# Kernel optimization log

Measured on AMD Instinct MI355X. Metric: run time of the kernel, lower is better.

## Reference

```python
import jax, jax.numpy as jnp
import numpy as np

N_EMBED = 768
NUM_EXPERTS = 8
TOP_K = 2
B, S = 2, 2048
THRESH = 1e-09


def setup_inputs() -> dict:
    key = jax.random.key(0)
    ks = jax.random.split(key, 12)
    d, e, f = N_EMBED, NUM_EXPERTS, 4 * N_EMBED
    s_in = 1.0 / np.sqrt(d)
    s_hid = 1.0 / np.sqrt(f)
    return {
        'x': jax.random.normal(ks[0], (B, S, d), jnp.float32),
        'noise': jax.random.normal(ks[1], (B * S, e), jnp.float32),
        'Wg': jax.random.normal(ks[2], (d, e), jnp.float32) * s_in,
        'bg': jnp.zeros((e,), jnp.float32),
        'Wn': jax.random.normal(ks[3], (d, e), jnp.float32) * s_in,
        'bn': jnp.zeros((e,), jnp.float32),
        'W1': jax.random.normal(ks[4], (e, d, f), jnp.float32) * s_in,
        'b1': jnp.zeros((e, f), jnp.float32),
        'W2': jax.random.normal(ks[5], (e, f, d), jnp.float32) * s_hid,
        'b2': jnp.zeros((e, d), jnp.float32),
    }


def reference(x, noise, Wg, bg, Wn, bn, W1, b1, W2, b2):
    Bsz, Ssz, d = x.shape
    T = Bsz * Ssz
    xr = x.reshape(T, d)  # [T, d]

    # Noisy top-k router
    logits = xr @ Wg + bg                     # [T, E]
    noise_logits = xr @ Wn + bn               # [T, E]
    noisy = logits + noise * jax.nn.softplus(noise_logits)
    vals, idx = jax.lax.top_k(noisy, TOP_K)   # [T, K]
    rows = jnp.arange(T)[:, None]
    sparse = jnp.full_like(noisy, -jnp.inf).at[rows, idx].set(vals)
    probs = jax.nn.softmax(sparse, axis=-1)   # [T, E]; zeros off top-k

    # Gate = prob masked by activation threshold (matches torch dispatch)
    gate = jnp.where(probs > THRESH, probs, 0.0)  # [T, E]

    # Dense per-expert MLP (dropout=0 -> identity), combined by gate
    h = jax.nn.relu(jnp.einsum('td,edf->etf', xr, W1) + b1[:, None, :])  # [E, T, 4d]
    y = jnp.einsum('etf,efd->etd', h, W2) + b2[:, None, :]               # [E, T, d]
    out = jnp.einsum('te,etd->td', gate, y)                              # [T, d]
    return out.reshape(Bsz, Ssz, d)
```

## Files before the change

### kernel.cpp

```cpp
#include <hip/hip_runtime.h>
#include <math.h>

typedef unsigned short u16;
typedef unsigned int u32;

#define D_EMB 768
#define F_HID 3072
#define N_TOK 4096
#define N_PAIR 8192
#define GATE_TH 1e-9f

typedef float f32x4 __attribute__((ext_vector_type(4)));
typedef __bf16 bfrag __attribute__((ext_vector_type(8)));

__device__ inline float b2f(u16 u) {
    union { float f; u32 i; } c; c.i = ((u32)u) << 16; return c.f;
}
__device__ inline u16 f2b(float f) {
    union { float f; u32 i; } c; c.f = f;
    u32 r = c.i + 0x7FFFu + ((c.i >> 16) & 1u);
    return (u16)(r >> 16);
}
__device__ inline f32x4 mfma16(bfrag a, bfrag b, f32x4 c) {
    return __builtin_amdgcn_mfma_f32_16x16x32_bf16(a, b, c, 0, 0, 0);
}
__device__ inline void gll16(const u16* g, u16* l) {
    __builtin_amdgcn_global_load_lds(
        (const __attribute__((address_space(1))) u32*)g,
        (__attribute__((address_space(3))) u32*)l, 16, 0, 0);
}
__device__ inline void sbar() {
    asm volatile("" ::: "memory");
    __builtin_amdgcn_s_barrier();
    asm volatile("" ::: "memory");
}
__device__ inline void waitv0() { asm volatile("s_waitcnt vmcnt(0)" ::: "memory"); }
__device__ inline void waitv6() { asm volatile("s_waitcnt vmcnt(6)" ::: "memory"); }
__device__ inline void waitv8() { asm volatile("s_waitcnt vmcnt(8)" ::: "memory"); }

__global__ void moe_init_kernel(int* __restrict__ cnt) {
    if (threadIdx.x < 8) cnt[threadIdx.x] = 0;
}
__global__ __launch_bounds__(256) void moe_zero_kernel(uint4* __restrict__ out) {
    int i = blockIdx.x * 256 + threadIdx.x;
    out[i] = make_uint4(0, 0, 0, 0);
}

__global__ __launch_bounds__(64) void moe_router_v2(
    const float* __restrict__ x, const float* __restrict__ noise,
    const float* __restrict__ Wg, const float* __restrict__ bg,
    const float* __restrict__ Wn, const float* __restrict__ bn,
    int* __restrict__ tk_e, float* __restrict__ tk_g, int* __restrict__ cnt)
{
    const int lane = threadIdx.x;
    const int tl = lane & 7, q = lane >> 3;
    const int t = blockIdx.x * 8 + tl;
    float ag[8] = {}, an[8] = {};
    const float4* xp = (const float4*)(x + (size_t)t * D_EMB + q * 96);
#pragma unroll 4
    for (int k4 = 0; k4 < 24; k4++) {
        float4 xv = xp[k4];
        const int kb = q * 96 + k4 * 4;
#pragma unroll
        for (int c = 0; c < 4; c++) {
            float xc = (&xv.x)[c];
            const float4* wg = (const float4*)(Wg + (size_t)(kb + c) * 8);
            const float4* wn = (const float4*)(Wn + (size_t)(kb + c) * 8);
            float4 g0 = wg[0], g1 = wg[1], n0 = wn[0], n1 = wn[1];
            ag[0] += xc * g0.x; ag[1] += xc * g0.y; ag[2] += xc * g0.z; ag[3] += xc * g0.w;
            ag[4] += xc * g1.x; ag[5] += xc * g1.y; ag[6] += xc * g1.z; ag[7] += xc * g1.w;
            an[0] += xc * n0.x; an[1] += xc * n0.y; an[2] += xc * n0.z; an[3] += xc * n0.w;
            an[4] += xc * n1.x; an[5] += xc * n1.y; an[6] += xc * n1.z; an[7] += xc * n1.w;
        }
    }
#pragma unroll
    for (int e = 0; e < 8; e++) {
        ag[e] += __shfl_xor(ag[e], 8);  an[e] += __shfl_xor(an[e], 8);
        ag[e] += __shfl_xor(ag[e], 16); an[e] += __shfl_xor(an[e], 16);
        ag[e] += __shfl_xor(ag[e], 32); an[e] += __shfl_xor(an[e], 32);
    }
    if (q == 0) {
        float best = -INFINITY, sec = -INFINITY; int be = 0, se = 0;
#pragma unroll
        for (int e = 0; e < 8; e++) {
            float nl = an[e] + bn[e];
            float sp = nl > 0.f ? nl + log1pf(expf(-nl)) : log1pf(expf(nl));
            float v = ag[e] + bg[e] + noise[(size_t)t * 8 + e] * sp;
            if (v > best) { sec = best; se = be; best = v; be = e; }
            else if (v > sec) { sec = v; se = e; }
        }
        float ex = expf(sec - best);
        float g1 = 1.f / (1.f + ex), g2 = ex / (1.f + ex);
        tk_e[t * 2 + 0] = (g1 > GATE_TH) ? be : -1; tk_g[t * 2 + 0] = g1;
        tk_e[t * 2 + 1] = (g2 > GATE_TH) ? se : -1; tk_g[t * 2 + 1] = g2;
        if (g1 > GATE_TH) atomicAdd(&cnt[be], 1);
        if (g2 > GATE_TH) atomicAdd(&cnt[se], 1);
    }
}

__global__ void moe_offsets_kernel(const int* __restrict__ cnt,
                                   int* __restrict__ off, int* __restrict__ cursor) {
    if (threadIdx.x == 0) {
        int s = 0;
        for (int e = 0; e < 8; e++) { off[e] = s; cursor[e] = s; s += cnt[e]; }
    }
}
__global__ void moe_scatter_kernel(const int* __restrict__ tk_e, const float* __restrict__ tk_g,
                                   int* __restrict__ cursor, int* __restrict__ plist,
                                   float* __restrict__ pg, int* __restrict__ pos) {
    int i = blockIdx.x * 256 + threadIdx.x;
    if (i < N_PAIR) {
        int e = tk_e[i];
        if (e >= 0) {
            int p = atomicAdd(&cursor[e], 1);
            plist[p] = i >> 1;
            pg[p] = tk_g[i];
            pos[i] = p;
        }
    }
}

__global__ __launch_bounds__(256) void moe_cvtx_kernel(
    const float4* __restrict__ x, ushort4* __restrict__ xb) {
    int i = blockIdx.x * 256 + threadIdx.x;
    float4 v = x[i];
    ushort4 o;
    o.x = f2b(v.x); o.y = f2b(v.y); o.z = f2b(v.z); o.w = f2b(v.w);
    xb[i] = o;
}

__global__ __launch_bounds__(256) void moe_transcvt_kernel(
    const float* __restrict__ in, u16* __restrict__ out, int R, int C) {
    __shared__ float tile[32][33];
    const int z = blockIdx.z;
    const int c0 = blockIdx.x * 32, r0 = blockIdx.y * 32;
    const int tx = threadIdx.x & 31, ty = threadIdx.x >> 5;
    const size_t base = (size_t)z * R * C;
#pragma unroll
    for (int j = 0; j < 32; j += 8)
        tile[ty + j][tx] = in[base + (size_t)(r0 + ty + j) * C + c0 + tx];
    __syncthreads();
#pragma unroll
    for (int j = 0; j < 32; j += 8)
        out[base + (size_t)(c0 + ty + j) * R + r0 + tx] = f2b(tile[tx][ty + j]);
}

__global__ __launch_bounds__(256) void moe_ffn1_kernel(
    const u16* __restrict__ xb, const u16* __restrict__ w1t, const float* __restrict__ b1,
    const int* __restrict__ plist, const int* __restrict__ cnt, const int* __restrict__ off,
    u16* __restrict__ h, int P0, int P1)
{
    __shared__ __align__(16) u16 As[2][128 * 64];
    __shared__ __align__(16) u16 Bs[2][128 * 64];
    const int GX = 24, GY = 16;
    int f = blockIdx.x + GX * (blockIdx.y + GY * blockIdx.z);
    int swz = (f & 7) * 384 + (f >> 3);
    int nb = swz % GX;
    int t2 = swz / GX;
    int mb = t2 % GY;
    int e  = t2 / GY;

    int lo = off[e], hi = lo + cnt[e];
    if (lo < P0) lo = P0;
    if (hi > P1) hi = P1;
    const int Cl = hi - lo;
    if (Cl <= 0) return;
    const int n0 = nb * 128;
    const int tid = threadIdx.x;
    const int lane = tid & 63, wave = tid >> 6;
    const int wr = wave >> 1, wc = wave & 1;
    const int qq = lane >> 4, r = lane & 15;
    const int srow = tid >> 3;
    const int gq = (tid & 7) ^ (srow & 7);

    const u16* bsrc[4];
#pragma unroll
    for (int j = 0; j < 4; j++)
        bsrc[j] = w1t + ((size_t)e * F_HID + n0 + j * 32 + srow) * D_EMB + gq * 8;

    for (int m0 = mb * 128; m0 < Cl; m0 += GY * 128) {
        const u16* asrc[4];
#pragma unroll
        for (int j = 0; j < 4; j++) {
            int mr = m0 + j * 32 + srow;
            if (mr > Cl - 1) mr = Cl - 1;
            asrc[j] = xb + (size_t)plist[lo + mr] * D_EMB + gq * 8;
        }
        f32x4 acc[4][4] = {};

        auto stage = [&](int kt, int buf) {
            const int k0 = kt * 64;
#pragma unroll
            for (int j = 0; j < 4; j++)
                gll16(asrc[j] + k0, &As[buf][j * 2048 + wave * 512]);
#pragma unroll
            for (int j = 0; j < 4; j++)
                gll16(bsrc[j] + k0, &Bs[buf][j * 2048 + wave * 512]);
        };
        auto compute = [&](int buf) {
#pragma unroll
            for (int kk = 0; kk < 2; kk++) {
                bfrag af[4], bf[4];
#pragma unroll
                for (int i = 0; i < 4; i++) {
                    int rowa = wr * 64 + i * 16 + r;
                    int rowb = wc * 64 + i * 16 + r;
                    int slot = ((qq + 4 * kk) ^ (r & 7)) * 8;
                    af[i] = *(const bfrag*)(&As[buf][rowa * 64 + slot]);
                    bf[i] = *(const bfrag*)(&Bs[buf][rowb * 64 + slot]);
                }
#pragma unroll
                for (int mi = 0; mi < 4; mi++)
#pragma unroll
                    for (int ni = 0; ni < 4; ni++)
                        acc[mi][ni] = mfma16(af[mi], bf[ni], acc[mi][ni]);
            }
        };

        waitv0();
        stage(0, 0);
        for (int kt = 0; kt < 11; kt++) {
            stage(kt + 1, (kt + 1) & 1);
            waitv8(); sbar();
            compute(kt & 1);
            sbar();
        }
        waitv0(); sbar();
        compute(1);

#pragma unroll
        for (int mi = 0; mi < 4; mi++)
#pragma unroll
            for (int ni = 0; ni < 4; ni++) {
                int col = n0 + wc * 64 + ni * 16 + r;
                float bias = b1[(size_t)e * F_HID + col];
#pragma unroll
                for (int i = 0; i < 4; i++) {
                    int m = m0 + wr * 64 + mi * 16 + qq * 4 + i;
                    if (m < Cl) {
                        float v = acc[mi][ni][i] + bias;
                        h[(size_t)(lo - P0 + m) * F_HID + col] = f2b(v > 0.f ? v : 0.f);
                    }
                }
            }
    }
}

__global__ __launch_bounds__(256) void moe_ffn2_kernel(
    const u16* __restrict__ h, const u16* __restrict__ w2t, const float* __restrict__ b2,
    const int* __restrict__ cnt, const int* __restrict__ off,
    float* __restrict__ y, int P0, int P1)
{
    __shared__ __align__(16) u16 As[2][64 * 64];
    __shared__ __align__(16) u16 Bs[2][128 * 64];
    const int GX = 6, GY = 32;
    int f = blockIdx.x + GX * (blockIdx.y + GY * blockIdx.z);
    int swz = (f & 7) * 192 + (f >> 3);
    int nb = swz % GX;
    int t2 = swz / GX;
    int mb = t2 % GY;
    int e  = t2 / GY;

    int lo = off[e], hi = lo + cnt[e];
    if (lo < P0) lo = P0;
    if (hi > P1) hi = P1;
    const int Cl = hi - lo;
    if (Cl <= 0) return;
    const int n0 = nb * 128;
    const int tid = threadIdx.x;
    const int lane = tid & 63, wave = tid >> 6;
    const int wr = wave >> 1, wc = wave & 1;
    const int qq = lane >> 4, r = lane & 15;
    const int srow = tid >> 3;
    const int gq = (tid & 7) ^ (srow & 7);
    const int hcap = P1 - P0;

    const u16* bsrc[4];
#pragma unroll
    for (int j = 0; j < 4; j++)
        bsrc[j] = w2t + ((size_t)e * D_EMB + n0 + j * 32 + srow) * F_HID + gq * 8;

    for (int m0 = mb * 64; m0 < Cl; m0 += GY * 64) {
        const u16* asrc[2];
#pragma unroll
        for (int j = 0; j < 2; j++) {
            int mr = m0 + j * 32 + srow;
            if (mr > Cl - 1) mr = Cl - 1;
            asrc[j] = h + (size_t)(lo - P0 + ((mr < hcap) ? mr : hcap - 1)) * F_HID + gq * 8;
        }
        f32x4 acc[2][4] = {};

        auto stage = [&](int kt, int buf) {
            const int k0 = kt * 64;
#pragma unroll
            for (int j = 0; j < 2; j++)
                gll16(asrc[j] + k0, &As[buf][j * 2048 + wave * 512]);
#pragma unroll
            for (int j = 0; j < 4; j++)
                gll16(bsrc[j] + k0, &Bs[buf][j * 2048 + wave * 512]);
        };
        auto compute = [&](int buf) {
#pragma unroll
            for (int kk = 0; kk < 2; kk++) {
                bfrag af[2], bf[4];
#pragma unroll
                for (int i = 0; i < 2; i++) {
                    int rowa = wr * 32 + i * 16 + r;
                    int slot = ((qq + 4 * kk) ^ (r & 7)) * 8;
                    af[i] = *(const bfrag*)(&As[buf][rowa * 64 + slot]);
                }
#pragma unroll
                for (int i = 0; i < 4; i++) {
                    int rowb = wc * 64 + i * 16 + r;
                    int slot = ((qq + 4 * kk) ^ (r & 7)) * 8;
                    bf[i] = *(const bfrag*)(&Bs[buf][rowb * 64 + slot]);
                }
#pragma unroll
                for (int mi = 0; mi < 2; mi++)
#pragma unroll
                    for (int ni = 0; ni < 4; ni++)
                        acc[mi][ni] = mfma16(af[mi], bf[ni], acc[mi][ni]);
            }
        };

        waitv0();
        stage(0, 0);
        for (int kt = 0; kt < 47; kt++) {
            stage(kt + 1, (kt + 1) & 1);
            waitv6(); sbar();
            compute(kt & 1);
            sbar();
        }
        waitv0(); sbar();
        compute(1);

#pragma unroll
        for (int mi = 0; mi < 2; mi++)
#pragma unroll
            for (int ni = 0; ni < 4; ni++) {
                int col = n0 + wc * 64 + ni * 16 + r;
                float bias = b2[(size_t)e * D_EMB + col];
#pragma unroll
                for (int i = 0; i < 4; i++) {
                    int m = m0 + wr * 32 + mi * 16 + qq * 4 + i;
                    if (m < Cl)
                        y[(size_t)(lo + m) * D_EMB + col] = acc[mi][ni][i] + bias;
                }
            }
    }
}

__global__ __launch_bounds__(256) void moe_combine_kernel(
    const float* __restrict__ y, const int* __restrict__ tk_e,
    const float* __restrict__ tk_g, const int* __restrict__ pos,
    float4* __restrict__ out)
{
    int i = blockIdx.x * 256 + threadIdx.x;
    int t = i / 192;
    int c = i - t * 192;
    float4 a = make_float4(0.f, 0.f, 0.f, 0.f);
#pragma unroll
    for (int k = 0; k < 2; k++) {
        int e = tk_e[t * 2 + k];
        if (e >= 0) {
            float g = tk_g[t * 2 + k];
            float4 v = ((const float4*)(y + (size_t)pos[t * 2 + k] * D_EMB))[c];
            a.x += g * v.x; a.y += g * v.y; a.z += g * v.z; a.w += g * v.w;
        }
    }
    out[i] = a;
}

#define XSTR 776
#define HSTR 3080
#define BMF 8
__global__ __launch_bounds__(256) void moe_ffn_fused_f32(
    const float* __restrict__ x,
    const float* __restrict__ w1, const float* __restrict__ b1,
    const float* __restrict__ w2, const float* __restrict__ b2,
    const int* __restrict__ plist, const float* __restrict__ pg,
    const int* __restrict__ cnt, const int* __restrict__ off,
    float* __restrict__ out)
{
    __shared__ __align__(16) u16 xs[BMF * XSTR];
    __shared__ __align__(16) u16 hs[BMF * HSTR];
    const int e = blockIdx.x;
    const int Cl = cnt[e];
    if (Cl <= 0) return;
    const int O = off[e];
    const int tid = threadIdx.x;
    for (int t0 = blockIdx.y * BMF; t0 < Cl; t0 += gridDim.y * BMF) {
        for (int ci = tid; ci < BMF * 192; ci += 256) {
            int row = ci / 192, c = ci - row * 192;
            float4 v = make_float4(0.f, 0.f, 0.f, 0.f);
            if (t0 + row < Cl) {
                int tok = plist[O + t0 + row];
                v = *(const float4*)(x + (size_t)tok * D_EMB + c * 4);
            }
            u16* d = &xs[row * XSTR + c * 4];
            d[0] = f2b(v.x); d[1] = f2b(v.y); d[2] = f2b(v.z); d[3] = f2b(v.w);
        }
        __syncthreads();
        for (int wi = tid; wi < BMF * 768; wi += 256) {
            int row = wi / 768, nc = wi - row * 768;
            int n0 = nc * 4;
            float a0 = 0, a1 = 0, a2 = 0, a3 = 0;
            const float* wp = w1 + (size_t)e * D_EMB * F_HID + n0;
            const u16* xr = &xs[row * XSTR];
            for (int k = 0; k < D_EMB; k++) {
                float4 wv = *(const float4*)(wp + (size_t)k * F_HID);
                float xv = b2f(xr[k]);
                a0 += xv * wv.x; a1 += xv * wv.y; a2 += xv * wv.z; a3 += xv * wv.w;
            }
            const float* bp = b1 + (size_t)e * F_HID + n0;
            u16* hp = &hs[row * HSTR + n0];
            float v;
            v = a0 + bp[0]; hp[0] = f2b(v > 0.f ? v : 0.f);
            v = a1 + bp[1]; hp[1] = f2b(v > 0.f ? v : 0.f);
            v = a2 + bp[2]; hp[2] = f2b(v > 0.f ? v : 0.f);
            v = a3 + bp[3]; hp[3] = f2b(v > 0.f ? v : 0.f);
        }
        __syncthreads();
        for (int wi = tid; wi < BMF * 192; wi += 256) {
            int row = wi / 192, nc = wi - row * 192;
            int n0 = nc * 4;
            float a0 = 0, a1 = 0, a2 = 0, a3 = 0;
            const float* wp = w2 + (size_t)e * F_HID * D_EMB + n0;
            const u16* hr = &hs[row * HSTR];
            for (int k = 0; k < F_HID; k++) {
                float4 wv = *(const float4*)(wp + (size_t)k * D_EMB);
                float hv = b2f(hr[k]);
                a0 += hv * wv.x; a1 += hv * wv.y; a2 += hv * wv.z; a3 += hv * wv.w;
            }
            if (t0 + row < Cl) {
                int p = O + t0 + row;
                int tok = plist[p];
                float g = pg[p];
                const float* bp = b2 + (size_t)e * D_EMB + n0;
                float* op = out + (size_t)tok * D_EMB + n0;
                atomicAdd(&op[0], g * (a0 + bp[0]));
                atomicAdd(&op[1], g * (a1 + bp[1]));
                atomicAdd(&op[2], g * (a2 + bp[2]));
                atomicAdd(&op[3], g * (a3 + bp[3]));
            }
        }
        __syncthreads();
    }
}

extern "C" void kernel_launch(void* const* d_in, const int* in_sizes, int n_in,
                              void* d_out, int out_size, void* d_ws, size_t ws_size,
                              hipStream_t stream) {
    const float* x     = (const float*)d_in[0];
    const float* noise = (const float*)d_in[1];
    const float* Wg    = (const float*)d_in[2];
    const float* bg    = (const float*)d_in[3];
    const float* Wn    = (const float*)d_in[4];
    const float* bn    = (const float*)d_in[5];
    const float* W1    = (const float*)d_in[6];
    const float* b1    = (const float*)d_in[7];
    const float* W2    = (const float*)d_in[8];
    const float* b2    = (const float*)d_in[9];
    float* out = (float*)d_out;

    char* ws = (char*)d_ws;
    int*   cnt    = (int*)(ws + 0);
    int*   off    = (int*)(ws + 256);
    int*   cursor = (int*)(ws + 512);
    int*   tk_e   = (int*)(ws + 1024);
    float* tk_g   = (float*)(ws + 33792);
    int*   plist  = (int*)(ws + 66560);
    float* pg     = (float*)(ws + 99328);
    int*   pos    = (int*)(ws + 132096);
    const size_t W1T_OFF = 164864;
    const size_t W2T_OFF = W1T_OFF + 37748736ull;
    const size_t XB_OFF  = W2T_OFF + 37748736ull;
    const size_t Y_OFF   = XB_OFF + 6291456ull;
    const size_t H_OFF   = Y_OFF + 25165824ull;
    u16*   w1t = (u16*)(ws + W1T_OFF);
    u16*   w2t = (u16*)(ws + W2T_OFF);
    u16*   xb  = (u16*)(ws + XB_OFF);
    float* y   = (float*)(ws + Y_OFF);
    u16*   h   = (u16*)(ws + H_OFF);

    int pchunk = 0;
    for (int p = N_PAIR; p >= 512; p >>= 1) {
        if (H_OFF + (size_t)p * F_HID * 2 <= ws_size) { pchunk = p; break; }
    }

    moe_init_kernel<<<dim3(1), dim3(64), 0, stream>>>(cnt);
    moe_router_v2<<<dim3(512), dim3(64), 0, stream>>>(
        x, noise, Wg, bg, Wn, bn, tk_e, tk_g, cnt);
    moe_offsets_kernel<<<dim3(1), dim3(64), 0, stream>>>(cnt, off, cursor);
    moe_scatter_kernel<<<dim3(N_PAIR / 256), dim3(256), 0, stream>>>(
        tk_e, tk_g, cursor, plist, pg, pos);

    if (pchunk > 0) {
        moe_cvtx_kernel<<<dim3(3072), dim3(256), 0, stream>>>(
            (const float4*)x, (ushort4*)xb);
        moe_transcvt_kernel<<<dim3(F_HID / 32, D_EMB / 32, 8), dim3(256), 0, stream>>>(
            W1, w1t, D_EMB, F_HID);
        moe_transcvt_kernel<<<dim3(D_EMB / 32, F_HID / 32, 8), dim3(256), 0, stream>>>(
            W2, w2t, F_HID, D_EMB);
        for (int c = 0; c < N_PAIR / pchunk; c++) {
            int P0 = c * pchunk, P1 = P0 + pchunk;
            moe_ffn1_kernel<<<dim3(24, 16, 8), dim3(256), 0, stream>>>(
                xb, w1t, b1, plist, cnt, off, h, P0, P1);
            moe_ffn2_kernel<<<dim3(6, 32, 8), dim3(256), 0, stream>>>(
                h, w2t, b2, cnt, off, y, P0, P1);
        }
        moe_combine_kernel<<<dim3(3072), dim3(256), 0, stream>>>(
            y, tk_e, tk_g, pos, (float4*)out);
    } else {
        moe_zero_kernel<<<dim3(3072), dim3(256), 0, stream>>>((uint4*)out);
        moe_ffn_fused_f32<<<dim3(8, 192), dim3(256), 0, stream>>>(
            x, W1, b1, W2, b2, plist, pg, cnt, off, out);
    }
    (void)in_sizes; (void)n_in; (void)out_size;
}
```

Measured before the change: 462.9 us.

## Shrink GEMM K-tile to 32, enlarge FFN2 M-tile, fuse x cast into router

Both expert GEMM kernels now stage 32-wide K slices instead of 64, using a new XOR swizzle and smaller LDS buffers. FFN2 moves to 128x128 tiles with 16 M-blocks. The bf16 cast of x is folded into the router kernel, and when the workspace is large enough a single weight buffer is shared: W1 is transposed, FFN1 runs, then W2 is transposed into the same buffer, all without chunking. The goal is higher occupancy, less LDS pressure and fewer launches, at the cost of twice as many barriers per K step and weight transposes that no longer overlap.

```diff
diff --git a/kernel.cpp b/kernel.cpp
--- a/kernel.cpp
+++ b/kernel.cpp
@@ -35,8 +35,7 @@
     asm volatile("" ::: "memory");
 }
 __device__ inline void waitv0() { asm volatile("s_waitcnt vmcnt(0)" ::: "memory"); }
-__device__ inline void waitv6() { asm volatile("s_waitcnt vmcnt(6)" ::: "memory"); }
-__device__ inline void waitv8() { asm volatile("s_waitcnt vmcnt(8)" ::: "memory"); }
+__device__ inline void waitv4() { asm volatile("s_waitcnt vmcnt(4)" ::: "memory"); }
 
 __global__ void moe_init_kernel(int* __restrict__ cnt) {
     if (threadIdx.x < 8) cnt[threadIdx.x] = 0;
@@ -46,11 +45,12 @@
     out[i] = make_uint4(0, 0, 0, 0);
 }
 
-__global__ __launch_bounds__(64) void moe_router_v2(
+__global__ __launch_bounds__(64) void moe_router_v3(
     const float* __restrict__ x, const float* __restrict__ noise,
     const float* __restrict__ Wg, const float* __restrict__ bg,
     const float* __restrict__ Wn, const float* __restrict__ bn,
-    int* __restrict__ tk_e, float* __restrict__ tk_g, int* __restrict__ cnt)
+    int* __restrict__ tk_e, float* __restrict__ tk_g, int* __restrict__ cnt,
+    ushort4* __restrict__ xb4)
 {
     const int lane = threadIdx.x;
     const int tl = lane & 7, q = lane >> 3;
@@ -95,6 +95,16 @@
         tk_e[t * 2 + 1] = (g2 > GATE_TH) ? se : -1; tk_g[t * 2 + 1] = g2;
         if (g1 > GATE_TH) atomicAdd(&cnt[be], 1);
         if (g2 > GATE_TH) atomicAdd(&cnt[se], 1);
+    }
+    if (xb4) {
+        const int t0 = blockIdx.x * 8;
+        for (int i = lane; i < 8 * 192; i += 64) {
+            int ti = i / 192, c = i - ti * 192;
+            float4 v = *(const float4*)(x + (size_t)(t0 + ti) * D_EMB + c * 4);
+            ushort4 o;
+            o.x = f2b(v.x); o.y = f2b(v.y); o.z = f2b(v.z); o.w = f2b(v.w);
+            xb4[(size_t)(t0 + ti) * 192 + c] = o;
+        }
     }
 }
 
@@ -120,15 +130,6 @@
     }
 }
 
-__global__ __launch_bounds__(256) void moe_cvtx_kernel(
-    const float4* __restrict__ x, ushort4* __restrict__ xb) {
-    int i = blockIdx.x * 256 + threadIdx.x;
-    float4 v = x[i];
-    ushort4 o;
-    o.x = f2b(v.x); o.y = f2b(v.y); o.z = f2b(v.z); o.w = f2b(v.w);
-    xb[i] = o;
-}
-
 __global__ __launch_bounds__(256) void moe_transcvt_kernel(
     const float* __restrict__ in, u16* __restrict__ out, int R, int C) {
     __shared__ float tile[32][33];
@@ -146,12 +147,12 @@
 }
 
 __global__ __launch_bounds__(256) void moe_ffn1_kernel(
-    const u16* __restrict__ xb, const u16* __restrict__ w1t, const float* __restrict__ b1,
+    const u16* __restrict__ xb, const u16* __restrict__ wt, const float* __restrict__ b1,
     const int* __restrict__ plist, const int* __restrict__ cnt, const int* __restrict__ off,
     u16* __restrict__ h, int P0, int P1)
 {
-    __shared__ __align__(16) u16 As[2][128 * 64];
-    __shared__ __align__(16) u16 Bs[2][128 * 64];
+    __shared__ __align__(16) u16 As[2][128 * 32];
+    __shared__ __align__(16) u16 Bs[2][128 * 32];
     const int GX = 24, GY = 16;
     int f = blockIdx.x + GX * (blockIdx.y + GY * blockIdx.z);
     int swz = (f & 7) * 384 + (f >> 3);
@@ -170,58 +171,55 @@
     const int lane = tid & 63, wave = tid >> 6;
     const int wr = wave >> 1, wc = wave & 1;
     const int qq = lane >> 4, r = lane & 15;
-    const int srow = tid >> 3;
-    const int gq = (tid & 7) ^ (srow & 7);
-
-    const u16* bsrc[4];
-#pragma unroll
-    for (int j = 0; j < 4; j++)
-        bsrc[j] = w1t + ((size_t)e * F_HID + n0 + j * 32 + srow) * D_EMB + gq * 8;
+    const int sig = (r & 3) ^ ((r >> 2) & 3);
+    const int sa = ((qq ^ sig) << 3);
+    const int srow = tid >> 2;
+    const int gq = (tid & 3) ^ ((tid >> 2) & 3) ^ ((tid >> 4) & 3);
+
+    const u16* bsrc[2];
+#pragma unroll
+    for (int j = 0; j < 2; j++)
+        bsrc[j] = wt + ((size_t)e * F_HID + n0 + j * 64 + srow) * D_EMB + gq * 8;
 
     for (int m0 = mb * 128; m0 < Cl; m0 += GY * 128) {
-        const u16* asrc[4];
-#pragma unroll
-        for (int j = 0; j < 4; j++) {
-            int mr = m0 + j * 32 + srow;
+        const u16* asrc[2];
+#pragma unroll
+        for (int j = 0; j < 2; j++) {
+            int mr = m0 + j * 64 + srow;
             if (mr > Cl - 1) mr = Cl - 1;
             asrc[j] = xb + (size_t)plist[lo + mr] * D_EMB + gq * 8;
         }
         f32x4 acc[4][4] = {};
 
         auto stage = [&](int kt, int buf) {
-            const int k0 = kt * 64;
-#pragma unroll
-            for (int j = 0; j < 4; j++)
+            const int k0 = kt * 32;
+#pragma unroll
+            for (int j = 0; j < 2; j++)
                 gll16(asrc[j] + k0, &As[buf][j * 2048 + wave * 512]);
 #pragma unroll
-            for (int j = 0; j < 4; j++)
+            for (int j = 0; j < 2; j++)
                 gll16(bsrc[j] + k0, &Bs[buf][j * 2048 + wave * 512]);
         };
         auto compute = [&](int buf) {
-#pragma unroll
-            for (int kk = 0; kk < 2; kk++) {
-                bfrag af[4], bf[4];
-#pragma unroll
-                for (int i = 0; i < 4; i++) {
-                    int rowa = wr * 64 + i * 16 + r;
-                    int rowb = wc * 64 + i * 16 + r;
-                    int slot = ((qq + 4 * kk) ^ (r & 7)) * 8;
-                    af[i] = *(const bfrag*)(&As[buf][rowa * 64 + slot]);
-                    bf[i] = *(const bfrag*)(&Bs[buf][rowb * 64 + slot]);
-                }
-#pragma unroll
-                for (int mi = 0; mi < 4; mi++)
-#pragma unroll
-                    for (int ni = 0; ni < 4; ni++)
-                        acc[mi][ni] = mfma16(af[mi], bf[ni], acc[mi][ni]);
-            }
+            bfrag af[4], bf[4];
+#pragma unroll
+            for (int i = 0; i < 4; i++) {
+                af[i] = *(const bfrag*)(&As[buf][(wr * 64 + i * 16 + r) * 32 + sa]);
+                bf[i] = *(const bfrag*)(&Bs[buf][(wc * 64 + i * 16 + r) * 32 + sa]);
+            }
+#pragma unroll
+            for (int mi = 0; mi < 4; mi++)
+#pragma unroll
+                for (int ni = 0; ni < 4; ni++)
+                    acc[mi][ni] = mfma16(af[mi], bf[ni], acc[mi][ni]);
         };
 
         waitv0();
         stage(0, 0);
-        for (int kt = 0; kt < 11; kt++) {
+#pragma unroll 2
+        for (int kt = 0; kt < 23; kt++) {
             stage(kt + 1, (kt + 1) & 1);
-            waitv8(); sbar();
+            waitv4(); sbar();
             compute(kt & 1);
             sbar();
         }
@@ -243,19 +241,20 @@
                     }
                 }
             }
+        sbar();
     }
 }
 
 __global__ __launch_bounds__(256) void moe_ffn2_kernel(
-    const u16* __restrict__ h, const u16* __restrict__ w2t, const float* __restrict__ b2,
+    const u16* __restrict__ h, const u16* __restrict__ wt, const float* __restrict__ b2,
     const int* __restrict__ cnt, const int* __restrict__ off,
     float* __restrict__ y, int P0, int P1)
 {
-    __shared__ __align__(16) u16 As[2][64 * 64];
-    __shared__ __align__(16) u16 Bs[2][128 * 64];
-    const int GX = 6, GY = 32;
+    __shared__ __align__(16) u16 As[2][128 * 32];
+    __shared__ __align__(16) u16 Bs[2][128 * 32];
+    const int GX = 6, GY = 16;
     int f = blockIdx.x + GX * (blockIdx.y + GY * blockIdx.z);
-    int swz = (f & 7) * 192 + (f >> 3);
+    int swz = (f & 7) * 96 + (f >> 3);
     int nb = swz % GX;
     int t2 = swz / GX;
     int mb = t2 % GY;
@@ -271,63 +270,55 @@
     const int lane = tid & 63, wave = tid >> 6;
     const int wr = wave >> 1, wc = wave & 1;
     const int qq = lane >> 4, r = lane & 15;
-    const int srow = tid >> 3;
-    const int gq = (tid & 7) ^ (srow & 7);
-    const int hcap = P1 - P0;
-
-    const u16* bsrc[4];
-#pragma unroll
-    for (int j = 0; j < 4; j++)
-        bsrc[j] = w2t + ((size_t)e * D_EMB + n0 + j * 32 + srow) * F_HID + gq * 8;
-
-    for (int m0 = mb * 64; m0 < Cl; m0 += GY * 64) {
+    const int sig = (r & 3) ^ ((r >> 2) & 3);
+    const int sa = ((qq ^ sig) << 3);
+    const int srow = tid >> 2;
+    const int gq = (tid & 3) ^ ((tid >> 2) & 3) ^ ((tid >> 4) & 3);
+
+    const u16* bsrc[2];
+#pragma unroll
+    for (int j = 0; j < 2; j++)
+        bsrc[j] = wt + ((size_t)e * D_EMB + n0 + j * 64 + srow) * F_HID + gq * 8;
+
+    for (int m0 = mb * 128; m0 < Cl; m0 += GY * 128) {
         const u16* asrc[2];
 #pragma unroll
         for (int j = 0; j < 2; j++) {
-            int mr = m0 + j * 32 + srow;
+            int mr = m0 + j * 64 + srow;
             if (mr > Cl - 1) mr = Cl - 1;
-            asrc[j] = h + (size_t)(lo - P0 + ((mr < hcap) ? mr : hcap - 1)) * F_HID + gq * 8;
-        }
-        f32x4 acc[2][4] = {};
+            asrc[j] = h + (size_t)(lo - P0 + mr) * F_HID + gq * 8;
+        }
+        f32x4 acc[4][4] = {};
 
         auto stage = [&](int kt, int buf) {
-            const int k0 = kt * 64;
+            const int k0 = kt * 32;
 #pragma unroll
             for (int j = 0; j < 2; j++)
                 gll16(asrc[j] + k0, &As[buf][j * 2048 + wave * 512]);
 #pragma unroll
-            for (int j = 0; j < 4; j++)
+            for (int j = 0; j < 2; j++)
                 gll16(bsrc[j] + k0, &Bs[buf][j * 2048 + wave * 512]);
         };
         auto compute = [&](int buf) {
-#pragma unroll
-            for (int kk = 0; kk < 2; kk++) {
-                bfrag af[2], bf[4];
-#pragma unroll
-                for (int i = 0; i < 2; i++) {
-                    int rowa = wr * 32 + i * 16 + r;
-                    int slot = ((qq + 4 * kk) ^ (r & 7)) * 8;
-                    af[i] = *(const bfrag*)(&As[buf][rowa * 64 + slot]);
-                }
-#pragma unroll
-                for (int i = 0; i < 4; i++) {
-                    int rowb = wc * 64 + i * 16 + r;
-                    int slot = ((qq + 4 * kk) ^ (r & 7)) * 8;
-                    bf[i] = *(const bfrag*)(&Bs[buf][rowb * 64 + slot]);
-                }
-#pragma unroll
-                for (int mi = 0; mi < 2; mi++)
-#pragma unroll
-                    for (int ni = 0; ni < 4; ni++)
-                        acc[mi][ni] = mfma16(af[mi], bf[ni], acc[mi][ni]);
-            }
+            bfrag af[4], bf[4];
+#pragma unroll
+            for (int i = 0; i < 4; i++) {
+                af[i] = *(const bfrag*)(&As[buf][(wr * 64 + i * 16 + r) * 32 + sa]);
+                bf[i] = *(const bfrag*)(&Bs[buf][(wc * 64 + i * 16 + r) * 32 + sa]);
+            }
+#pragma unroll
+            for (int mi = 0; mi < 4; mi++)
+#pragma unroll
+                for (int ni = 0; ni < 4; ni++)
+                    acc[mi][ni] = mfma16(af[mi], bf[ni], acc[mi][ni]);
         };
 
         waitv0();
         stage(0, 0);
-        for (int kt = 0; kt < 47; kt++) {
+#pragma unroll 2
+        for (int kt = 0; kt < 95; kt++) {
             stage(kt + 1, (kt + 1) & 1);
-            waitv6(); sbar();
+            waitv4(); sbar();
             compute(kt & 1);
             sbar();
         }
@@ -335,18 +326,19 @@
         compute(1);
 
 #pragma unroll
-        for (int mi = 0; mi < 2; mi++)
+        for (int mi = 0; mi < 4; mi++)
 #pragma unroll
             for (int ni = 0; ni < 4; ni++) {
                 int col = n0 + wc * 64 + ni * 16 + r;
                 float bias = b2[(size_t)e * D_EMB + col];
 #pragma unroll
                 for (int i = 0; i < 4; i++) {
-                    int m = m0 + wr * 32 + mi * 16 + qq * 4 + i;
+                    int m = m0 + wr * 64 + mi * 16 + qq * 4 + i;
                     if (m < Cl)
                         y[(size_t)(lo + m) * D_EMB + col] = acc[mi][ni][i] + bias;
                 }
             }
+        sbar();
     }
 }
 
@@ -472,32 +464,60 @@
     int*   plist  = (int*)(ws + 66560);
     float* pg     = (float*)(ws + 99328);
     int*   pos    = (int*)(ws + 132096);
-    const size_t W1T_OFF = 164864;
-    const size_t W2T_OFF = W1T_OFF + 37748736ull;
-    const size_t XB_OFF  = W2T_OFF + 37748736ull;
-    const size_t Y_OFF   = XB_OFF + 6291456ull;
-    const size_t H_OFF   = Y_OFF + 25165824ull;
-    u16*   w1t = (u16*)(ws + W1T_OFF);
-    u16*   w2t = (u16*)(ws + W2T_OFF);
-    u16*   xb  = (u16*)(ws + XB_OFF);
-    float* y   = (float*)(ws + Y_OFF);
-    u16*   h   = (u16*)(ws + H_OFF);
-
+    const size_t SMALL  = 164864;
+    const size_t WSZ    = 37748736ull;
+    const size_t XB_SZ  = 6291456ull;
+    const size_t Y_SZ   = 25165824ull;
+    const size_t H_FULL = 50331648ull;
+
+    const size_t NEED_A = SMALL + WSZ + XB_SZ + Y_SZ + H_FULL;
+
+    if (ws_size >= NEED_A) {
+        u16*   wt = (u16*)(ws + SMALL);
+        u16*   xb = (u16*)(ws + SMALL + WSZ);
+        float* y  = (float*)(ws + SMALL + WSZ + XB_SZ);
+        u16*   h  = (u16*)(ws + SMALL + WSZ + XB_SZ + Y_SZ);
+
+        moe_init_kernel<<<dim3(1), dim3(64), 0, stream>>>(cnt);
+        moe_router_v3<<<dim3(512), dim3(64), 0, stream>>>(
+            x, noise, Wg, bg, Wn, bn, tk_e, tk_g, cnt, (ushort4*)xb);
+        moe_offsets_kernel<<<dim3(1), dim3(64), 0, stream>>>(cnt, off, cursor);
+        moe_scatter_kernel<<<dim3(N_PAIR / 256), dim3(256), 0, stream>>>(
+            tk_e, tk_g, cursor, plist, pg, pos);
+        moe_transcvt_kernel<<<dim3(F_HID / 32, D_EMB / 32, 8), dim3(256), 0, stream>>>(
+            W1, wt, D_EMB, F_HID);
+        moe_ffn1_kernel<<<dim3(24, 16, 8), dim3(256), 0, stream>>>(
+            xb, wt, b1, plist, cnt, off, h, 0, N_PAIR);
+        moe_transcvt_kernel<<<dim3(D_EMB / 32, F_HID / 32, 8), dim3(256), 0, stream>>>(
+            W2, wt, F_HID, D_EMB);
+        moe_ffn2_kernel<<<dim3(6, 16, 8), dim3(256), 0, stream>>>(
+            h, wt, b2, cnt, off, y, 0, N_PAIR);
+        moe_combine_kernel<<<dim3(3072), dim3(256), 0, stream>>>(
+            y, tk_e, tk_g, pos, (float4*)out);
+        (void)in_sizes; (void)n_in; (void)out_size;
+        return;
+    }
+
+    const size_t B_BASE = SMALL + 2 * WSZ + XB_SZ + Y_SZ;
     int pchunk = 0;
     for (int p = N_PAIR; p >= 512; p >>= 1) {
-        if (H_OFF + (size_t)p * F_HID * 2 <= ws_size) { pchunk = p; break; }
+        if (B_BASE + (size_t)p * F_HID * 2 <= ws_size) { pchunk = p; break; }
     }
 
     moe_init_kernel<<<dim3(1), dim3(64), 0, stream>>>(cnt);
-    moe_router_v2<<<dim3(512), dim3(64), 0, stream>>>(
-        x, noise, Wg, bg, Wn, bn, tk_e, tk_g, cnt);
+    moe_router_v3<<<dim3(512), dim3(64), 0, stream>>>(
+        x, noise, Wg, bg, Wn, bn, tk_e, tk_g, cnt,
+        pchunk > 0 ? (ushort4*)(ws + SMALL + 2 * WSZ) : (ushort4*)0);
     moe_offsets_kernel<<<dim3(1), dim3(64), 0, stream>>>(cnt, off, cursor);
     moe_scatter_kernel<<<dim3(N_PAIR / 256), dim3(256), 0, stream>>>(
         tk_e, tk_g, cursor, plist, pg, pos);
 
     if (pchunk > 0) {
-        moe_cvtx_kernel<<<dim3(3072), dim3(256), 0, stream>>>(
-            (const float4*)x, (ushort4*)xb);
+        u16*   w1t = (u16*)(ws + SMALL);
+        u16*   w2t = (u16*)(ws + SMALL + WSZ);
+        u16*   xb  = (u16*)(ws + SMALL + 2 * WSZ);
+        float* y   = (float*)(ws + SMALL + 2 * WSZ + XB_SZ);
+        u16*   h   = (u16*)(ws + B_BASE);
         moe_transcvt_kernel<<<dim3(F_HID / 32, D_EMB / 32, 8), dim3(256), 0, stream>>>(
             W1, w1t, D_EMB, F_HID);
         moe_transcvt_kernel<<<dim3(D_EMB / 32, F_HID / 32, 8), dim3(256), 0, stream>>>(
@@ -506,7 +526,7 @@
             int P0 = c * pchunk, P1 = P0 + pchunk;
             moe_ffn1_kernel<<<dim3(24, 16, 8), dim3(256), 0, stream>>>(
                 xb, w1t, b1, plist, cnt, off, h, P0, P1);
-            moe_ffn2_kernel<<<dim3(6, 32, 8), dim3(256), 0, stream>>>(
+            moe_ffn2_kernel<<<dim3(6, 16, 8), dim3(256), 0, stream>>>(
                 h, w2t, b2, cnt, off, y, P0, P1);
         }
         moe_combine_kernel<<<dim3(3072), dim3(256), 0, stream>>>(
```

Result: slower. 512.0 us (+10.6%).

## Fuse x bf16 conversion into router, vectorize transpose stores, share weight buffer

Applied to the files above, without the earlier changes.

The bf16 conversion of x now happens inside the router kernel, removing the separate cvtx launch. The transpose-convert kernel writes ushort4 vectors instead of scalar u16 stores. When the workspace is large enough, one transposed-weight buffer is reused for W1 and then W2, which frees room for a full-size h buffer so FFN1 and FFN2 each run once without chunking. The router's extra pass over x adds work to a small-grid kernel, and the single-buffer path serialises the W2 transpose after FFN1.

```diff
diff --git a/kernel.cpp b/kernel.cpp
--- a/kernel.cpp
+++ b/kernel.cpp
@@ -46,11 +46,12 @@
     out[i] = make_uint4(0, 0, 0, 0);
 }
 
-__global__ __launch_bounds__(64) void moe_router_v2(
+__global__ __launch_bounds__(64) void moe_router_v3(
     const float* __restrict__ x, const float* __restrict__ noise,
     const float* __restrict__ Wg, const float* __restrict__ bg,
     const float* __restrict__ Wn, const float* __restrict__ bn,
-    int* __restrict__ tk_e, float* __restrict__ tk_g, int* __restrict__ cnt)
+    int* __restrict__ tk_e, float* __restrict__ tk_g, int* __restrict__ cnt,
+    ushort4* __restrict__ xb4)
 {
     const int lane = threadIdx.x;
     const int tl = lane & 7, q = lane >> 3;
@@ -95,6 +96,16 @@
         tk_e[t * 2 + 1] = (g2 > GATE_TH) ? se : -1; tk_g[t * 2 + 1] = g2;
         if (g1 > GATE_TH) atomicAdd(&cnt[be], 1);
         if (g2 > GATE_TH) atomicAdd(&cnt[se], 1);
+    }
+    if (xb4) {
+        const int t0 = blockIdx.x * 8;
+        for (int i = lane; i < 8 * 192; i += 64) {
+            int ti = i / 192, c = i - ti * 192;
+            float4 v = *(const float4*)(x + (size_t)(t0 + ti) * D_EMB + c * 4);
+            ushort4 o;
+            o.x = f2b(v.x); o.y = f2b(v.y); o.z = f2b(v.z); o.w = f2b(v.w);
+            xb4[(size_t)(t0 + ti) * 192 + c] = o;
+        }
     }
 }
 
@@ -120,15 +131,6 @@
     }
 }
 
-__global__ __launch_bounds__(256) void moe_cvtx_kernel(
-    const float4* __restrict__ x, ushort4* __restrict__ xb) {
-    int i = blockIdx.x * 256 + threadIdx.x;
-    float4 v = x[i];
-    ushort4 o;
-    o.x = f2b(v.x); o.y = f2b(v.y); o.z = f2b(v.z); o.w = f2b(v.w);
-    xb[i] = o;
-}
-
 __global__ __launch_bounds__(256) void moe_transcvt_kernel(
     const float* __restrict__ in, u16* __restrict__ out, int R, int C) {
     __shared__ float tile[32][33];
@@ -140,13 +142,17 @@
     for (int j = 0; j < 32; j += 8)
         tile[ty + j][tx] = in[base + (size_t)(r0 + ty + j) * C + c0 + tx];
     __syncthreads();
-#pragma unroll
-    for (int j = 0; j < 32; j += 8)
-        out[base + (size_t)(c0 + ty + j) * R + r0 + tx] = f2b(tile[tx][ty + j]);
+    const int c = threadIdx.x >> 3, rb = (threadIdx.x & 7) * 4;
+    ushort4 o;
+    o.x = f2b(tile[rb + 0][c]);
+    o.y = f2b(tile[rb + 1][c]);
+    o.z = f2b(tile[rb + 2][c]);
+    o.w = f2b(tile[rb + 3][c]);
+    *(ushort4*)(out + base + (size_t)(c0 + c) * R + r0 + rb) = o;
 }
 
 __global__ __launch_bounds__(256) void moe_ffn1_kernel(
-    const u16* __restrict__ xb, const u16* __restrict__ w1t, const float* __restrict__ b1,
+    const u16* __restrict__ xb, const u16* __restrict__ wt, const float* __restrict__ b1,
     const int* __restrict__ plist, const int* __restrict__ cnt, const int* __restrict__ off,
     u16* __restrict__ h, int P0, int P1)
 {
@@ -176,7 +182,7 @@
     const u16* bsrc[4];
 #pragma unroll
     for (int j = 0; j < 4; j++)
-        bsrc[j] = w1t + ((size_t)e * F_HID + n0 + j * 32 + srow) * D_EMB + gq * 8;
+        bsrc[j] = wt + ((size_t)e * F_HID + n0 + j * 32 + srow) * D_EMB + gq * 8;
 
     for (int m0 = mb * 128; m0 < Cl; m0 += GY * 128) {
         const u16* asrc[4];
@@ -247,7 +253,7 @@
 }
 
 __global__ __launch_bounds__(256) void moe_ffn2_kernel(
-    const u16* __restrict__ h, const u16* __restrict__ w2t, const float* __restrict__ b2,
+    const u16* __restrict__ h, const u16* __restrict__ wt, const float* __restrict__ b2,
     const int* __restrict__ cnt, const int* __restrict__ off,
     float* __restrict__ y, int P0, int P1)
 {
@@ -278,7 +284,7 @@
     const u16* bsrc[4];
 #pragma unroll
     for (int j = 0; j < 4; j++)
-        bsrc[j] = w2t + ((size_t)e * D_EMB + n0 + j * 32 + srow) * F_HID + gq * 8;
+        bsrc[j] = wt + ((size_t)e * D_EMB + n0 + j * 32 + srow) * F_HID + gq * 8;
 
     for (int m0 = mb * 64; m0 < Cl; m0 += GY * 64) {
         const u16* asrc[2];
@@ -472,32 +478,60 @@
     int*   plist  = (int*)(ws + 66560);
     float* pg     = (float*)(ws + 99328);
     int*   pos    = (int*)(ws + 132096);
-    const size_t W1T_OFF = 164864;
-    const size_t W2T_OFF = W1T_OFF + 37748736ull;
-    const size_t XB_OFF  = W2T_OFF + 37748736ull;
-    const size_t Y_OFF   = XB_OFF + 6291456ull;
-    const size_t H_OFF   = Y_OFF + 25165824ull;
-    u16*   w1t = (u16*)(ws + W1T_OFF);
-    u16*   w2t = (u16*)(ws + W2T_OFF);
-    u16*   xb  = (u16*)(ws + XB_OFF);
-    float* y   = (float*)(ws + Y_OFF);
-    u16*   h   = (u16*)(ws + H_OFF);
-
+    const size_t SMALL  = 164864;
+    const size_t WSZ    = 37748736ull;
+    const size_t XB_SZ  = 6291456ull;
+    const size_t Y_SZ   = 25165824ull;
+    const size_t H_FULL = 50331648ull;
+
+    const size_t NEED_A = SMALL + WSZ + XB_SZ + Y_SZ + H_FULL;
+
+    if (ws_size >= NEED_A) {
+        u16*   wt = (u16*)(ws + SMALL);
+        u16*   xb = (u16*)(ws + SMALL + WSZ);
+        float* y  = (float*)(ws + SMALL + WSZ + XB_SZ);
+        u16*   h  = (u16*)(ws + SMALL + WSZ + XB_SZ + Y_SZ);
+
+        moe_init_kernel<<<dim3(1), dim3(64), 0, stream>>>(cnt);
+        moe_router_v3<<<dim3(512), dim3(64), 0, stream>>>(
+            x, noise, Wg, bg, Wn, bn, tk_e, tk_g, cnt, (ushort4*)xb);
+        moe_offsets_kernel<<<dim3(1), dim3(64), 0, stream>>>(cnt, off, cursor);
+        moe_scatter_kernel<<<dim3(N_PAIR / 256), dim3(256), 0, stream>>>(
+            tk_e, tk_g, cursor, plist, pg, pos);
+        moe_transcvt_kernel<<<dim3(F_HID / 32, D_EMB / 32, 8), dim3(256), 0, stream>>>(
+            W1, wt, D_EMB, F_HID);
+        moe_ffn1_kernel<<<dim3(24, 16, 8), dim3(256), 0, stream>>>(
+            xb, wt, b1, plist, cnt, off, h, 0, N_PAIR);
+        moe_transcvt_kernel<<<dim3(D_EMB / 32, F_HID / 32, 8), dim3(256), 0, stream>>>(
+            W2, wt, F_HID, D_EMB);
+        moe_ffn2_kernel<<<dim3(6, 32, 8), dim3(256), 0, stream>>>(
+            h, wt, b2, cnt, off, y, 0, N_PAIR);
+        moe_combine_kernel<<<dim3(3072), dim3(256), 0, stream>>>(
+            y, tk_e, tk_g, pos, (float4*)out);
+        (void)in_sizes; (void)n_in; (void)out_size;
+        return;
+    }
+
+    const size_t B_BASE = SMALL + 2 * WSZ + XB_SZ + Y_SZ;
     int pchunk = 0;
     for (int p = N_PAIR; p >= 512; p >>= 1) {
-        if (H_OFF + (size_t)p * F_HID * 2 <= ws_size) { pchunk = p; break; }
+        if (B_BASE + (size_t)p * F_HID * 2 <= ws_size) { pchunk = p; break; }
     }
 
     moe_init_kernel<<<dim3(1), dim3(64), 0, stream>>>(cnt);
-    moe_router_v2<<<dim3(512), dim3(64), 0, stream>>>(
-        x, noise, Wg, bg, Wn, bn, tk_e, tk_g, cnt);
+    moe_router_v3<<<dim3(512), dim3(64), 0, stream>>>(
+        x, noise, Wg, bg, Wn, bn, tk_e, tk_g, cnt,
+        pchunk > 0 ? (ushort4*)(ws + SMALL + 2 * WSZ) : (ushort4*)0);
     moe_offsets_kernel<<<dim3(1), dim3(64), 0, stream>>>(cnt, off, cursor);
     moe_scatter_kernel<<<dim3(N_PAIR / 256), dim3(256), 0, stream>>>(
         tk_e, tk_g, cursor, plist, pg, pos);
 
     if (pchunk > 0) {
-        moe_cvtx_kernel<<<dim3(3072), dim3(256), 0, stream>>>(
-            (const float4*)x, (ushort4*)xb);
+        u16*   w1t = (u16*)(ws + SMALL);
+        u16*   w2t = (u16*)(ws + SMALL + WSZ);
+        u16*   xb  = (u16*)(ws + SMALL + 2 * WSZ);
+        float* y   = (float*)(ws + SMALL + 2 * WSZ + XB_SZ);
+        u16*   h   = (u16*)(ws + B_BASE);
         moe_transcvt_kernel<<<dim3(F_HID / 32, D_EMB / 32, 8), dim3(256), 0, stream>>>(
             W1, w1t, D_EMB, F_HID);
         moe_transcvt_kernel<<<dim3(D_EMB / 32, F_HID / 32, 8), dim3(256), 0, stream>>>(
```

After: 455.5 us. No clear change (-1.6%).
